# Kernel tuning notes

Measured on AMD Instinct MI355X. Metric: run time of the kernel, lower is better.

Reference implementation:

```python
import jax, jax.numpy as jnp
import numpy as np

OBS_DIM, ACT_DIM, LATENT_DIM, BELIEF_DIM, T = 128, 32, 512, 1024, 32768


def setup_inputs() -> dict:
    key = jax.random.key(0)
    ks = jax.random.split(key, 8)
    s_ih = 1.0 / np.sqrt(BELIEF_DIM)
    s_enc = 1.0 / np.sqrt(OBS_DIM)
    return {
        "obs_seq": jax.random.normal(ks[0], (T, OBS_DIM), jnp.float32),
        "act_seq": jax.random.normal(ks[1], (T, ACT_DIM), jnp.float32),
        "enc_w": jax.random.uniform(ks[2], (LATENT_DIM, OBS_DIM), jnp.float32, -s_enc, s_enc),
        "enc_b": jax.random.uniform(ks[3], (LATENT_DIM,), jnp.float32, -s_enc, s_enc),
        "w_ih": jax.random.uniform(ks[4], (3 * BELIEF_DIM, LATENT_DIM + ACT_DIM), jnp.float32, -s_ih, s_ih),
        "w_hh": jax.random.uniform(ks[5], (3 * BELIEF_DIM, BELIEF_DIM), jnp.float32, -s_ih, s_ih),
        "b_ih": jax.random.uniform(ks[6], (3 * BELIEF_DIM,), jnp.float32, -s_ih, s_ih),
        "b_hh": jax.random.uniform(ks[7], (3 * BELIEF_DIM,), jnp.float32, -s_ih, s_ih),
    }


def reference(obs_seq, act_seq, enc_w, enc_b, w_ih, w_hh, b_ih, b_hh):
    H = w_hh.shape[1]
    # Encoder over all timesteps at once: (T, latent)
    z_seq = jnp.tanh(obs_seq @ enc_w.T + enc_b)
    # a_prev[t] = act_seq[t-1], zeros at t=0
    a_prev = jnp.concatenate(
        [jnp.zeros((1, act_seq.shape[1]), act_seq.dtype), act_seq[:-1]], axis=0)
    x_seq = jnp.concatenate([z_seq, a_prev], axis=-1)  # (T, latent+act)
    # Precompute input-side gate projections as one big GEMM: (T, 3H)
    gi_seq = x_seq @ w_ih.T + b_ih

    def step(h, gi_t):
        gh = w_hh @ h + b_hh  # (3H,)
        ir, iz, inn = jnp.split(gi_t, 3)
        hr, hz, hn = jnp.split(gh, 3)
        r = jax.nn.sigmoid(ir + hr)
        z = jax.nn.sigmoid(iz + hz)
        n = jnp.tanh(inn + r * hn)
        h_new = (1.0 - z) * n + z * h
        return h_new, h_new

    h0 = jnp.zeros((H,), x_seq.dtype)
    _, beliefs = jax.lax.scan(step, h0, gi_seq)
    return beliefs  # (T, belief_dim)
```

## Files before the change

kernel.cpp:

```cpp
#include <hip/hip_runtime.h>
#include <stdint.h>

#define T_STEPS 32768
#define HDIM    1024
#define LDIM    512
#define ADIM    32
#define NWG     128
#define NOUT    8

__global__ __launch_bounds__(256) void encoder_kernel(
    const float* __restrict__ obs,
    const float* __restrict__ w,
    const float* __restrict__ b,
    float* __restrict__ z)
{
    __shared__ float As[64][65];
    __shared__ float Bs[64][65];

    const int tile_n = blockIdx.x;
    const int tile_t = blockIdx.y;
    const int tid = threadIdx.x;
    const int ty = tid >> 4;
    const int tx = tid & 15;

    float acc[4][4] = {};

    for (int kt = 0; kt < 2; ++kt) {
        #pragma unroll
        for (int it = 0; it < 4; ++it) {
            int lin = it * 1024 + tid * 4;
            int r = lin >> 6, c = lin & 63;
            float4 va = *(const float4*)&obs[(size_t)(tile_t * 64 + r) * 128 + kt * 64 + c];
            As[r][c] = va.x; As[r][c+1] = va.y; As[r][c+2] = va.z; As[r][c+3] = va.w;
            float4 vb = *(const float4*)&w[(size_t)(tile_n * 64 + r) * 128 + kt * 64 + c];
            Bs[r][c] = vb.x; Bs[r][c+1] = vb.y; Bs[r][c+2] = vb.z; Bs[r][c+3] = vb.w;
        }
        __syncthreads();

        for (int k = 0; k < 64; ++k) {
            float av[4], bv[4];
            #pragma unroll
            for (int a = 0; a < 4; ++a) av[a] = As[ty * 4 + a][k];
            #pragma unroll
            for (int c = 0; c < 4; ++c) bv[c] = Bs[tx * 4 + c][k];
            #pragma unroll
            for (int a = 0; a < 4; ++a)
                #pragma unroll
                for (int c = 0; c < 4; ++c)
                    acc[a][c] = fmaf(av[a], bv[c], acc[a][c]);
        }
        __syncthreads();
    }

    #pragma unroll
    for (int a = 0; a < 4; ++a) {
        int row = tile_t * 64 + ty * 4 + a;
        #pragma unroll
        for (int c = 0; c < 4; ++c) {
            int col = tile_n * 64 + tx * 4 + c;
            z[(size_t)row * LDIM + col] = tanhf(acc[a][c] + b[col]);
        }
    }
}

__global__ __launch_bounds__(256, 1) void gru_kernel(
    float* __restrict__ out,
    const float* __restrict__ z_seq,
    const float* __restrict__ act,
    const float* __restrict__ w_ih,
    const float* __restrict__ w_hh,
    const float* __restrict__ b_ih,
    const float* __restrict__ b_hh,
    uint64_t* __restrict__ hbuf)
{
    __shared__ float h_lds[HDIM];
    __shared__ float z_lds[LDIM];
    __shared__ float a_lds[ADIM];
    __shared__ float h_pub[NOUT];

    const int tid  = threadIdx.x;
    const int wg   = blockIdx.x;
    const int grp  = tid >> 5;
    const int lane = tid & 31;
    const int i    = wg * NOUT + grp;

    float whr[32], whz[32], whn[32];
    {
        const float* pr = &w_hh[(size_t)i * HDIM + lane];
        const float* pz = &w_hh[(size_t)(HDIM + i) * HDIM + lane];
        const float* pn = &w_hh[(size_t)(2 * HDIM + i) * HDIM + lane];
        #pragma unroll
        for (int j = 0; j < 32; ++j) {
            whr[j] = pr[32 * j]; whz[j] = pz[32 * j]; whn[j] = pn[32 * j];
        }
    }
    float wir[17], wiz[17], win[17];
    {
        const float* pr = &w_ih[(size_t)i * 544 + lane];
        const float* pz = &w_ih[(size_t)(HDIM + i) * 544 + lane];
        const float* pn = &w_ih[(size_t)(2 * HDIM + i) * 544 + lane];
        #pragma unroll
        for (int j = 0; j < 17; ++j) {
            wir[j] = pr[32 * j]; wiz[j] = pz[32 * j]; win[j] = pn[32 * j];
        }
    }
    #pragma unroll
    for (int j = 0; j < 32; ++j) {
        asm volatile("" : "+v"(whr[j]), "+v"(whz[j]), "+v"(whn[j]));
    }
    #pragma unroll
    for (int j = 0; j < 17; ++j) {
        asm volatile("" : "+v"(wir[j]), "+v"(wiz[j]), "+v"(win[j]));
    }

    const float bir  = b_ih[i], biz = b_ih[HDIM + i], bin_ = b_ih[2 * HDIM + i];
    const float bhr  = b_hh[i], bhz = b_hh[HDIM + i], bhn  = b_hh[2 * HDIM + i];

    for (int q = tid; q < HDIM; q += 256) h_lds[q] = 0.0f;
    __syncthreads();

    for (int t = 0; t < T_STEPS; ++t) {
        if (tid < 128) {
            float4 v = *(const float4*)&z_seq[(size_t)t * LDIM + tid * 4];
            *(float4*)&z_lds[tid * 4] = v;
            if (tid < ADIM) {
                a_lds[tid] = (t == 0) ? 0.0f : act[(size_t)(t - 1) * ADIM + tid];
            }
        } else if (t > 0) {
            const int q = tid - 128;
            const uint64_t* bp = hbuf + ((size_t)((t - 1) & 1)) * HDIM + q * 8;
            const uint32_t want = (uint32_t)t;
            uint64_t v[8];
            int done = 0;
            while (done != 0xFF) {
                #pragma unroll
                for (int k = 0; k < 8; ++k) {
                    if (!(done & (1 << k))) {
                        v[k] = __hip_atomic_load(bp + k, __ATOMIC_RELAXED,
                                                 __HIP_MEMORY_SCOPE_AGENT);
                    }
                }
                #pragma unroll
                for (int k = 0; k < 8; ++k) {
                    if (!(done & (1 << k)) && (uint32_t)(v[k] >> 32) == want)
                        done |= (1 << k);
                }
            }
            float4 h0, h1;
            h0.x = __uint_as_float((uint32_t)v[0]);
            h0.y = __uint_as_float((uint32_t)v[1]);
            h0.z = __uint_as_float((uint32_t)v[2]);
            h0.w = __uint_as_float((uint32_t)v[3]);
            h1.x = __uint_as_float((uint32_t)v[4]);
            h1.y = __uint_as_float((uint32_t)v[5]);
            h1.z = __uint_as_float((uint32_t)v[6]);
            h1.w = __uint_as_float((uint32_t)v[7]);
            *(float4*)&h_lds[q * 8]     = h0;
            *(float4*)&h_lds[q * 8 + 4] = h1;
        }
        __syncthreads();

        float sr = 0.f, sz = 0.f, sn = 0.f;
        #pragma unroll
        for (int j = 0; j < 32; ++j) {
            float hv = h_lds[lane + 32 * j];
            sr = fmaf(whr[j], hv, sr);
            sz = fmaf(whz[j], hv, sz);
            sn = fmaf(whn[j], hv, sn);
        }
        float gr = 0.f, gz = 0.f, gn = 0.f;
        #pragma unroll
        for (int j = 0; j < 16; ++j) {
            float xv = z_lds[lane + 32 * j];
            gr = fmaf(wir[j], xv, gr);
            gz = fmaf(wiz[j], xv, gz);
            gn = fmaf(win[j], xv, gn);
        }
        {
            float xa = a_lds[lane];
            gr = fmaf(wir[16], xa, gr);
            gz = fmaf(wiz[16], xa, gz);
            gn = fmaf(win[16], xa, gn);
        }

        float vr = sr + gr, vz = sz + gz;
        #pragma unroll
        for (int m = 16; m >= 1; m >>= 1) {
            vr += __shfl_xor(vr, m);
            vz += __shfl_xor(vz, m);
            sn += __shfl_xor(sn, m);
            gn += __shfl_xor(gn, m);
        }

        if (lane == 0) {
            float r  = 1.0f / (1.0f + expf(-(vr + bir + bhr)));
            float zg = 1.0f / (1.0f + expf(-(vz + biz + bhz)));
            float n  = tanhf(gn + bin_ + r * (sn + bhn));
            float hold = h_lds[i];
            h_pub[grp] = (1.0f - zg) * n + zg * hold;
        }
        __syncthreads();

        if (tid < NOUT) {
            uint64_t pk = ((uint64_t)(uint32_t)(t + 1) << 32) |
                          (uint64_t)__float_as_uint(h_pub[tid]);
            __hip_atomic_store(&hbuf[((size_t)(t & 1)) * HDIM + wg * NOUT + tid],
                               pk, __ATOMIC_RELAXED, __HIP_MEMORY_SCOPE_AGENT);
        } else if (tid == NOUT) {
            float4 o0 = *(const float4*)&h_pub[0];
            float4 o1 = *(const float4*)&h_pub[4];
            *(float4*)&out[(size_t)t * HDIM + wg * NOUT]     = o0;
            *(float4*)&out[(size_t)t * HDIM + wg * NOUT + 4] = o1;
        }
    }
}

extern "C" void kernel_launch(void* const* d_in, const int* in_sizes, int n_in,
                              void* d_out, int out_size, void* d_ws, size_t ws_size,
                              hipStream_t stream) {
    const float* obs   = (const float*)d_in[0];
    const float* act   = (const float*)d_in[1];
    const float* enc_w = (const float*)d_in[2];
    const float* enc_b = (const float*)d_in[3];
    const float* w_ih  = (const float*)d_in[4];
    const float* w_hh  = (const float*)d_in[5];
    const float* b_ih  = (const float*)d_in[6];
    const float* b_hh  = (const float*)d_in[7];
    float* out = (float*)d_out;

    uint64_t* hbuf  = (uint64_t*)d_ws;
    float*    z_seq = (float*)((char*)d_ws + 65536);

    hipMemsetAsync(hbuf, 0, 2 * HDIM * sizeof(uint64_t), stream);

    encoder_kernel<<<dim3(8, 512), 256, 0, stream>>>(obs, enc_w, enc_b, z_seq);

    void* args[] = {(void*)&out, (void*)&z_seq, (void*)&act, (void*)&w_ih,
                    (void*)&w_hh, (void*)&b_ih, (void*)&b_hh, (void*)&hbuf};
    hipLaunchCooperativeKernel((void*)gru_kernel, dim3(NWG), dim3(256),
                               args, 0, stream);
}
```

Measured before the change: 94.40 ms.

## Halve GRU workgroups, double-buffer encoder inputs, add sleep to hidden-state polling

The recurrent kernel now runs 64 workgroups of 512 threads, each owning 16 hidden units instead of 8. The next timestep's encoder output and action are prefetched into double-buffered shared memory, so those global loads overlap with the current step. The polling loop on published hidden states adds s_sleep between retries to reduce memory traffic. The risk is that launch_bounds(512,2) caps registers well below the roughly 147 weight registers each thread holds. That can force spills, and fitting more waves per CU can lengthen each step's critical path.

```diff
diff --git a/kernel.cpp b/kernel.cpp
--- a/kernel.cpp
+++ b/kernel.cpp
@@ -5,8 +5,9 @@
 #define HDIM    1024
 #define LDIM    512
 #define ADIM    32
-#define NWG     128
-#define NOUT    8
+#define NWG     64
+#define NTHR    512
+#define NOUT    16
 
 __global__ __launch_bounds__(256) void encoder_kernel(
     const float* __restrict__ obs,
@@ -63,7 +64,7 @@
     }
 }
 
-__global__ __launch_bounds__(256, 1) void gru_kernel(
+__global__ __launch_bounds__(NTHR, 2) void gru_kernel(
     float* __restrict__ out,
     const float* __restrict__ z_seq,
     const float* __restrict__ act,
@@ -74,8 +75,8 @@
     uint64_t* __restrict__ hbuf)
 {
     __shared__ float h_lds[HDIM];
-    __shared__ float z_lds[LDIM];
-    __shared__ float a_lds[ADIM];
+    __shared__ float z_lds[2][LDIM];
+    __shared__ float a_lds[2][ADIM];
     __shared__ float h_pub[NOUT];
 
     const int tid  = threadIdx.x;
@@ -116,18 +117,26 @@
     const float bir  = b_ih[i], biz = b_ih[HDIM + i], bin_ = b_ih[2 * HDIM + i];
     const float bhr  = b_hh[i], bhz = b_hh[HDIM + i], bhn  = b_hh[2 * HDIM + i];
 
-    for (int q = tid; q < HDIM; q += 256) h_lds[q] = 0.0f;
+    for (int q = tid; q < HDIM; q += NTHR) h_lds[q] = 0.0f;
+    if (tid < 128) {
+        float4 v = *(const float4*)&z_seq[tid * 4];
+        *(float4*)&z_lds[0][tid * 4] = v;
+    }
+    if (tid < ADIM) a_lds[0][tid] = 0.0f;
     __syncthreads();
 
     for (int t = 0; t < T_STEPS; ++t) {
+        const int cur = t & 1, nxt = cur ^ 1;
+
+        float4 zpre;
+        float4 apre;
         if (tid < 128) {
-            float4 v = *(const float4*)&z_seq[(size_t)t * LDIM + tid * 4];
-            *(float4*)&z_lds[tid * 4] = v;
-            if (tid < ADIM) {
-                a_lds[tid] = (t == 0) ? 0.0f : act[(size_t)(t - 1) * ADIM + tid];
-            }
-        } else if (t > 0) {
-            const int q = tid - 128;
+            int tn = (t + 1 < T_STEPS) ? (t + 1) : t;
+            zpre = *(const float4*)&z_seq[(size_t)tn * LDIM + tid * 4];
+        } else if (tid < 136) {
+            apre = *(const float4*)&act[(size_t)t * ADIM + (tid - 128) * 4];
+        } else if (tid >= 256 && tid < 384 && t > 0) {
+            const int q = tid - 256;
             const uint64_t* bp = hbuf + ((size_t)((t - 1) & 1)) * HDIM + q * 8;
             const uint32_t want = (uint32_t)t;
             uint64_t v[8];
@@ -145,6 +154,7 @@
                     if (!(done & (1 << k)) && (uint32_t)(v[k] >> 32) == want)
                         done |= (1 << k);
                 }
+                if (done != 0xFF) __builtin_amdgcn_s_sleep(1);
             }
             float4 h0, h1;
             h0.x = __uint_as_float((uint32_t)v[0]);
@@ -171,13 +181,13 @@
         float gr = 0.f, gz = 0.f, gn = 0.f;
         #pragma unroll
         for (int j = 0; j < 16; ++j) {
-            float xv = z_lds[lane + 32 * j];
+            float xv = z_lds[cur][lane + 32 * j];
             gr = fmaf(wir[j], xv, gr);
             gz = fmaf(wiz[j], xv, gz);
             gn = fmaf(win[j], xv, gn);
         }
         {
-            float xa = a_lds[lane];
+            float xa = a_lds[cur][lane];
             gr = fmaf(wir[16], xa, gr);
             gz = fmaf(wiz[16], xa, gz);
             gn = fmaf(win[16], xa, gn);
@@ -204,13 +214,17 @@
         if (tid < NOUT) {
             uint64_t pk = ((uint64_t)(uint32_t)(t + 1) << 32) |
                           (uint64_t)__float_as_uint(h_pub[tid]);
-            __hip_atomic_store(&hbuf[((size_t)(t & 1)) * HDIM + wg * NOUT + tid],
+            __hip_atomic_store(&hbuf[(size_t)cur * HDIM + wg * NOUT + tid],
                                pk, __ATOMIC_RELAXED, __HIP_MEMORY_SCOPE_AGENT);
-        } else if (tid == NOUT) {
-            float4 o0 = *(const float4*)&h_pub[0];
-            float4 o1 = *(const float4*)&h_pub[4];
-            *(float4*)&out[(size_t)t * HDIM + wg * NOUT]     = o0;
-            *(float4*)&out[(size_t)t * HDIM + wg * NOUT + 4] = o1;
+        } else if (tid >= 32 && tid < 32 + NOUT) {
+            out[(size_t)t * HDIM + wg * NOUT + (tid - 32)] = h_pub[tid - 32];
+        } else if (tid < 32) {
+        }
+
+        if (tid < 128) {
+            *(float4*)&z_lds[nxt][tid * 4] = zpre;
+        } else if (tid < 136) {
+            *(float4*)&a_lds[nxt][(tid - 128) * 4] = apre;
         }
     }
 }
@@ -237,6 +251,6 @@
 
     void* args[] = {(void*)&out, (void*)&z_seq, (void*)&act, (void*)&w_ih,
                     (void*)&w_hh, (void*)&b_ih, (void*)&b_hh, (void*)&hbuf};
-    hipLaunchCooperativeKernel((void*)gru_kernel, dim3(NWG), dim3(256),
+    hipLaunchCooperativeKernel((void*)gru_kernel, dim3(NWG), dim3(NTHR),
                                args, 0, stream);
 }
```

Result: slower. 107.6 ms (+14.0%).
